# Kernel tuning notes

Hardware: AMD Instinct MI355X
Metric: run time of the kernel (lower is better)

The kernel has to match this reference:

```python
import jax, jax.numpy as jnp
import numpy as np
from jax.scipy.special import digamma, polygamma

N_ITERS = 100
TOL = 1e-3


def setup_inputs() -> dict:
    key = jax.random.key(0)
    x = jax.random.normal(key, (2_000_000, 10), dtype=jnp.float32)
    return {"x": x}


def reference(x):
    # x: [n, C] logits -> Dirichlet MLE over softmax probabilities
    p = jax.nn.softmax(x, axis=-1)            # [n, C]
    n = p.shape[0]
    m1 = p.mean(0)                            # [C] E[p]
    m2 = (p ** 2).mean(0)                     # [C] E[p^2]
    # method-of-moments initialization (as in the torch module)
    a0 = m1 * ((m1 - m2) / (m2 - m1 ** 2)).mean(-1)
    # loop-invariant sufficient statistic
    log_p_avg = jnp.log(p).mean(0)            # [C]

    def cond(carry):
        a, k, diff = carry
        return jnp.logical_and(k < N_ITERS, diff >= TOL)

    def body(carry):
        a, k, _ = carry
        g = (digamma(a.sum(-1)) - digamma(a) + log_p_avg) * n
        q = -n * polygamma(1, a)
        z = n * polygamma(1, a.sum(-1))
        q_inv = 1.0 / q
        b = (g * q_inv).sum(-1) / (1.0 / z + q_inv.sum(-1))
        a_new = a - (g - b) / q               # Newton step with rank-1 Hessian inverse
        diff = jnp.abs(a_new - a).sum()       # L1 norm, matches torch.norm(.,1)
        return (a_new, k + 1, diff)

    a, _, _ = jax.lax.while_loop(
        cond, body, (a0, jnp.int32(0), jnp.float32(jnp.inf))
    )
    return a.astype(jnp.float32)
```

## Files before the change

### kernel.cpp

```cpp
#include <hip/hip_runtime.h>
#include <math.h>

#define C 10
#define BLOCK 256
#define NBLOCKS 1024
#define WROWS 128
#define NSTATS (3 * C)

typedef float f4 __attribute__((ext_vector_type(4), aligned(4)));
typedef float f2 __attribute__((ext_vector_type(2), aligned(4)));


__device__ __forceinline__ void accum10(f4 r0, f4 r1, f2 r2,
                                        float* __restrict__ s1,
                                        float* __restrict__ s2,
                                        float* __restrict__ sl) {
  float v[C];
  v[0] = r0.x; v[1] = r0.y; v[2] = r0.z; v[3] = r0.w;
  v[4] = r1.x; v[5] = r1.y; v[6] = r1.z; v[7] = r1.w;
  v[8] = r2.x; v[9] = r2.y;
  float mx = v[0];
#pragma unroll
  for (int c = 1; c < C; c++) mx = fmaxf(mx, v[c]);
  float e[C], se = 0.f;
#pragma unroll
  for (int c = 0; c < C; c++) { v[c] -= mx; e[c] = __expf(v[c]); se += e[c]; }
  float inv = 1.0f / se;
  float lse = __logf(se);
#pragma unroll
  for (int c = 0; c < C; c++) {
    float p = e[c] * inv;
    s1[c] += p;
    s2[c] = fmaf(p, p, s2[c]);
    sl[c] += v[c] - lse;
  }
}


__global__ __launch_bounds__(BLOCK) void dir_stats_kernel(
    const float* __restrict__ x, float* __restrict__ partials,
    int nrows, int nblocks) {
  __shared__ float red[4][NSTATS];
  const int tid = threadIdx.x;
  const int lane = tid & 63;
  const int wave = tid >> 6;

  const int gwave = blockIdx.x * 4 + wave;
  const int wstride = nblocks * 4;
  const int ntiles = nrows / WROWS;
  const int tailStart = ntiles * WROWS;

  float s1[C], s2[C], sl[C];
#pragma unroll
  for (int c = 0; c < C; c++) { s1[c] = 0.f; s2[c] = 0.f; sl[c] = 0.f; }

  int g = gwave;
  f4 a0 = 0, a1 = 0, b0 = 0, b1 = 0, n0 = 0, n1 = 0, m0 = 0, m1 = 0;
  f2 a2 = 0, b2 = 0, n2 = 0, m2 = 0;
  if (g < ntiles) {
    const float* p = x + ((size_t)g * WROWS + lane) * C;
    a0 = *(const f4*)(p);       a1 = *(const f4*)(p + 4);   a2 = *(const f2*)(p + 8);
    b0 = *(const f4*)(p + 640); b1 = *(const f4*)(p + 644); b2 = *(const f2*)(p + 648);
  }
  while (g < ntiles) {
    const int gn = g + wstride;
    if (gn < ntiles) {
      const float* p = x + ((size_t)gn * WROWS + lane) * C;
      n0 = *(const f4*)(p);       n1 = *(const f4*)(p + 4);   n2 = *(const f2*)(p + 8);
      m0 = *(const f4*)(p + 640); m1 = *(const f4*)(p + 644); m2 = *(const f2*)(p + 648);
    }
    accum10(a0, a1, a2, s1, s2, sl);
    accum10(b0, b1, b2, s1, s2, sl);
    a0 = n0; a1 = n1; a2 = n2;
    b0 = m0; b1 = m1; b2 = m2;
    g = gn;
  }

  if (gwave == wstride - 1) {
    for (int rr = tailStart + lane; rr < nrows; rr += 64) {
      const float* r = x + (size_t)rr * C;
      f4 t0 = *(const f4*)(r);
      f4 t1 = *(const f4*)(r + 4);
      f2 t2 = *(const f2*)(r + 8);
      accum10(t0, t1, t2, s1, s2, sl);
    }
  }

#pragma unroll
  for (int c = 0; c < C; c++) {
    float v1 = s1[c], v2 = s2[c], v3 = sl[c];
#pragma unroll
    for (int off = 32; off >= 1; off >>= 1) {
      v1 += __shfl_down(v1, off);
      v2 += __shfl_down(v2, off);
      v3 += __shfl_down(v3, off);
    }
    if (lane == 0) {
      red[wave][c] = v1;
      red[wave][C + c] = v2;
      red[wave][2 * C + c] = v3;
    }
  }
  __syncthreads();
  if (tid < NSTATS) {
    float tot = red[0][tid] + red[1][tid] + red[2][tid] + red[3][tid];
    partials[(size_t)tid * nblocks + blockIdx.x] = tot;
  }
}


__device__ __forceinline__ double frcp(double x) {
  double r;
  asm("v_rcp_f64 %0, %1" : "=v"(r) : "v"(x));
  double e = fma(-x, r, 1.0);
  r = fma(r, e, r);
  e = fma(-x, r, 1.0);
  r = fma(r, e, r);
  return r;
}


__device__ __forceinline__ void digtri8(double x, double& dg, double& tg) {
  double i0 = frcp(x),       i1 = frcp(x + 1.0);
  double i2 = frcp(x + 2.0), i3 = frcp(x + 3.0);
  double i4 = frcp(x + 4.0), i5 = frcp(x + 5.0);
  double i6 = frcp(x + 6.0), i7 = frcp(x + 7.0);
  double rd = (i0 + i1) + (i2 + i3) + ((i4 + i5) + (i6 + i7));
  double rt = (i0 * i0 + i1 * i1) + (i2 * i2 + i3 * i3) +
              ((i4 * i4 + i5 * i5) + (i6 * i6 + i7 * i7));
  double y = x + 8.0;
  double yi = frcp(y), f = yi * yi;
  dg = log(y) - 0.5 * yi
     - f * (1.0 / 12 - f * (1.0 / 120 - f * (1.0 / 252 - f * (1.0 / 240 - f * (1.0 / 132)))))
     - rd;
  tg = rt + yi + 0.5 * f
     + f * yi * (1.0 / 6 - f * (1.0 / 30 - f * (1.0 / 42 - f * (1.0 / 30))));
}

__device__ __forceinline__ double wsum16(double v) {
#pragma unroll
  for (int off = 1; off < 16; off <<= 1) v += __shfl_xor(v, off);
  return v;
}


__global__ __launch_bounds__(1024) void dir_newton_kernel(
    const float* __restrict__ partials, float* __restrict__ out,
    int nparts, double nrows) {
  __shared__ double tot[NSTATS];
  const int tid = threadIdx.x;

  {
    const int j = tid >> 5;
    const int k = tid & 31;
    double s = 0.0;
    if (j < NSTATS) {
      const float* __restrict__ base = partials + (size_t)j * nparts;
      const int nv4 = nparts >> 2;
      const f4* __restrict__ b4 = (const f4*)base;
      for (int b = k; b < nv4; b += 32) {
        f4 v = b4[b];
        s += ((double)v.x + (double)v.y) + ((double)v.z + (double)v.w);
      }
      for (int b = (nv4 << 2) + k; b < nparts; b += 32)
        s += (double)base[b];
    }
#pragma unroll
    for (int off = 16; off >= 1; off >>= 1) s += __shfl_xor(s, off);
    if (j < NSTATS && k == 0) tot[j] = s;
  }
  __syncthreads();

  if (tid < 16) {
    const int c = tid;
    const bool act = (c < C);
    const double n = nrows;
    const double ninv = frcp(n);
    double m1 = 0.0, m2 = 0.0, lpa = 0.0;
    if (act) {
      m1 = tot[c] * ninv;
      m2 = tot[C + c] * ninv;
      lpa = tot[2 * C + c] * ninv;
    }
    double ratio = act ? (m1 - m2) * frcp(m2 - m1 * m1) : 0.0;
    double rmean = wsum16(ratio) * (1.0 / (double)C);
    double a = act ? m1 * rmean : 0.0;

    double diff = 1e30;
    for (int k = 0; k < 100 && diff >= 1e-3; k++) {
      double S = wsum16(a);
      double dgl, tgl;
      digtri8(act ? a : S, dgl, tgl);
      double dgS = __shfl(dgl, 10);
      double tgS = __shfl(tgl, 10);
      double g = act ? (dgS - dgl + lpa) * n : 0.0;
      double qinv = act ? -frcp(n * tgl) : 0.0;
      double z = n * tgS;
      double num = wsum16(g * qinv);
      double sq = wsum16(qinv);
      double b = num * z * frcp(fma(z, sq, 1.0));
      double anew = act ? a - (g - b) * qinv : 0.0;
      diff = wsum16(fabs(anew - a));
      a = anew;
    }
    if (act) out[c] = (float)a;
  }
}


extern "C" void kernel_launch(void* const* d_in, const int* in_sizes, int n_in,
                              void* d_out, int out_size, void* d_ws, size_t ws_size,
                              hipStream_t stream) {
  const float* x = (const float*)d_in[0];
  const int total = in_sizes[0];
  const int nrows = total / C;

  int grid = NBLOCKS;
  size_t need = (size_t)NSTATS * grid * sizeof(float);
  if (need > ws_size) {
    grid = (int)(ws_size / (NSTATS * sizeof(float)));
    if (grid < 1) grid = 1;
  }

  float* partials = (float*)d_ws;
  dir_stats_kernel<<<grid, BLOCK, 0, stream>>>(x, partials, nrows, grid);
  dir_newton_kernel<<<1, 1024, 0, stream>>>(partials, (float*)d_out, grid, (double)nrows);
}
```

Before: 119.4 us.

## Use DPP row reductions, readlane broadcasts and custom log in Newton loop

```diff
diff --git a/kernel.cpp b/kernel.cpp
--- a/kernel.cpp
+++ b/kernel.cpp
@@ -119,6 +119,63 @@
   return r;
 }
 
+template <int CTRL>
+__device__ __forceinline__ double dpp_rot(double v) {
+  long long l = __double_as_longlong(v);
+  int lo = (int)(unsigned)(l & 0xFFFFFFFFu);
+  int hi = (int)(unsigned)((unsigned long long)l >> 32);
+  lo = __builtin_amdgcn_update_dpp(0, lo, CTRL, 0xF, 0xF, true);
+  hi = __builtin_amdgcn_update_dpp(0, hi, CTRL, 0xF, 0xF, true);
+  return __longlong_as_double(((long long)(unsigned)lo) |
+                              ((long long)(unsigned)hi << 32));
+}
+
+__device__ __forceinline__ double wsum16d(double v) {
+  v += dpp_rot<0x121>(v);
+  v += dpp_rot<0x122>(v);
+  v += dpp_rot<0x124>(v);
+  v += dpp_rot<0x128>(v);
+  return v;
+}
+
+__device__ __forceinline__ double bcast10(double v) {
+  long long l = __double_as_longlong(v);
+  int lo = __builtin_amdgcn_readlane((int)(unsigned)(l & 0xFFFFFFFFu), 10);
+  int hi = __builtin_amdgcn_readlane((int)(unsigned)((unsigned long long)l >> 32), 10);
+  return __longlong_as_double(((long long)(unsigned)lo) |
+                              ((long long)(unsigned)hi << 32));
+}
+
+__device__ __forceinline__ double uni(double v) {
+  long long l = __double_as_longlong(v);
+  int lo = __builtin_amdgcn_readfirstlane((int)(unsigned)(l & 0xFFFFFFFFu));
+  int hi = __builtin_amdgcn_readfirstlane((int)(unsigned)((unsigned long long)l >> 32));
+  return __longlong_as_double(((long long)(unsigned)lo) |
+                              ((long long)(unsigned)hi << 32));
+}
+
+__device__ __forceinline__ double flog(double x) {
+  long long b = __double_as_longlong(x);
+  int e = (int)((b >> 52) & 0x7FF) - 1023;
+  double m = __longlong_as_double((b & 0x000FFFFFFFFFFFFFLL) | 0x3FF0000000000000LL);
+  int big = m > 1.4142135623730951;
+  m = big ? 0.5 * m : m;
+  e += big;
+  double f = (m - 1.0) * frcp(m + 1.0);
+  double f2 = f * f;
+  double f4_ = f2 * f2, f8_ = f4_ * f4_;
+  double p01 = fma(f2, 1.0 / 3,  1.0);
+  double p23 = fma(f2, 1.0 / 7,  1.0 / 5);
+  double p45 = fma(f2, 1.0 / 11, 1.0 / 9);
+  double p67 = fma(f2, 1.0 / 15, 1.0 / 13);
+  double p89 = fma(f2, 1.0 / 19, 1.0 / 17);
+  double q0 = fma(f4_, p23, p01);
+  double q1 = fma(f4_, p67, p45);
+  double q2 = fma(f4_, 1.0 / 21, p89);
+  double r0 = fma(f8_, q1, q0);
+  double p  = fma(f8_ * f8_, q2, r0);
+  return fma((double)e, 0.6931471805599453, 2.0 * f * p);
+}
 
 __device__ __forceinline__ void digtri8(double x, double& dg, double& tg) {
   double i0 = frcp(x),       i1 = frcp(x + 1.0);
@@ -130,17 +187,11 @@
               ((i4 * i4 + i5 * i5) + (i6 * i6 + i7 * i7));
   double y = x + 8.0;
   double yi = frcp(y), f = yi * yi;
-  dg = log(y) - 0.5 * yi
+  dg = flog(y) - 0.5 * yi
      - f * (1.0 / 12 - f * (1.0 / 120 - f * (1.0 / 252 - f * (1.0 / 240 - f * (1.0 / 132)))))
      - rd;
   tg = rt + yi + 0.5 * f
      + f * yi * (1.0 / 6 - f * (1.0 / 30 - f * (1.0 / 42 - f * (1.0 / 30))));
-}
-
-__device__ __forceinline__ double wsum16(double v) {
-#pragma unroll
-  for (int off = 1; off < 16; off <<= 1) v += __shfl_xor(v, off);
-  return v;
 }
 
 
@@ -183,25 +234,26 @@
       lpa = tot[2 * C + c] * ninv;
     }
     double ratio = act ? (m1 - m2) * frcp(m2 - m1 * m1) : 0.0;
-    double rmean = wsum16(ratio) * (1.0 / (double)C);
+    double rmean = wsum16d(ratio) * (1.0 / (double)C);
     double a = act ? m1 * rmean : 0.0;
 
+    double S = wsum16d(a);
     double diff = 1e30;
     for (int k = 0; k < 100 && diff >= 1e-3; k++) {
-      double S = wsum16(a);
       double dgl, tgl;
       digtri8(act ? a : S, dgl, tgl);
-      double dgS = __shfl(dgl, 10);
-      double tgS = __shfl(tgl, 10);
+      double dgS = bcast10(dgl);
+      double tgS = bcast10(tgl);
       double g = act ? (dgS - dgl + lpa) * n : 0.0;
       double qinv = act ? -frcp(n * tgl) : 0.0;
       double z = n * tgS;
-      double num = wsum16(g * qinv);
-      double sq = wsum16(qinv);
+      double num = wsum16d(g * qinv);
+      double sq  = wsum16d(qinv);
       double b = num * z * frcp(fma(z, sq, 1.0));
-      double anew = act ? a - (g - b) * qinv : 0.0;
-      diff = wsum16(fabs(anew - a));
-      a = anew;
+      double step = act ? (g - b) * qinv : 0.0;
+      a -= step;
+      S -= wsum16d(step);
+      diff = uni(wsum16d(fabs(step)));
     }
     if (act) out[c] = (float)a;
   }
```

Measured after the change: 118.9 us (median of 2 runs). Within noise of the previous version (-0.4%).
